# Optimization experiments

Hardware: AMD Instinct MI355X
Metric: run time of the kernel (lower is better)

Reference implementation:

```python
import jax, jax.numpy as jnp
from jax import lax
import numpy as np

I, H = 512, 1024
B, T = 64, 512


def setup_inputs() -> dict:
    key = jax.random.key(0)
    ks = jax.random.split(key, 16)
    p = lambda k, shape: (jax.random.normal(k, shape, dtype=jnp.float32) * 0.01)
    inp = {
        "inputs": jax.random.normal(ks[0], (B, T, I), dtype=jnp.float32),
        "h_prev_forward": jnp.zeros((B, H), dtype=jnp.float32),
        "h_prev_backward": jnp.zeros((B, H), dtype=jnp.float32),
        # forward-direction params
        "W_hr_f": p(ks[1], (H, H)), "W_xr_f": p(ks[2], (I, H)), "b_r_f": jnp.zeros((H,), jnp.float32),
        "W_hz_f": p(ks[3], (H, H)), "W_xz_f": p(ks[4], (I, H)), "b_z_f": jnp.zeros((H,), jnp.float32),
        "W_hh_f": p(ks[5], (H, H)), "W_xh_f": p(ks[6], (I, H)), "b_h_f": jnp.zeros((H,), jnp.float32),
        # backward-direction params
        "W_hr_b": p(ks[7], (H, H)), "W_xr_b": p(ks[8], (I, H)), "b_r_b": jnp.zeros((H,), jnp.float32),
        "W_hz_b": p(ks[9], (H, H)), "W_xz_b": p(ks[10], (I, H)), "b_z_b": jnp.zeros((H,), jnp.float32),
        "W_hh_b": p(ks[11], (H, H)), "W_xh_b": p(ks[12], (I, H)), "b_h_b": jnp.zeros((H,), jnp.float32),
    }
    return inp


def _gru_dir(x, h0, W_hr, W_xr, b_r, W_hz, W_xz, b_z, W_hh, W_xh, b_h, reverse):
    # Precompute input projections as big GEMMs: (B,T,I)@(I,H) -> (B,T,H)
    xr = jnp.einsum("bti,ih->bth", x, W_xr) + b_r
    xz = jnp.einsum("bti,ih->bth", x, W_xz) + b_z
    xh = jnp.einsum("bti,ih->bth", x, W_xh) + b_h
    # time-major for scan
    xs = (xr.transpose(1, 0, 2), xz.transpose(1, 0, 2), xh.transpose(1, 0, 2))

    def step(h, x_t):
        xr_t, xz_t, xh_t = x_t
        R = jax.nn.sigmoid(h @ W_hr + xr_t)
        Z = jax.nn.sigmoid(h @ W_hz + xz_t)
        # NOTE: original torch code computes (R * h) @ W_hh (left-to-right precedence)
        h_til = jnp.tanh((R * h) @ W_hh + xh_t)
        h_new = Z * h_til + (1.0 - Z) * h
        return h_new, h_new

    _, hs = lax.scan(step, h0, xs, reverse=reverse)  # hs: (T,B,H), time order preserved
    return hs.transpose(1, 0, 2)  # (B,T,H)


def reference(inputs, h_prev_forward, h_prev_backward,
              W_hr_f, W_xr_f, b_r_f, W_hz_f, W_xz_f, b_z_f, W_hh_f, W_xh_f, b_h_f,
              W_hr_b, W_xr_b, b_r_b, W_hz_b, W_xz_b, b_z_b, W_hh_b, W_xh_b, b_h_b):
    h_f = _gru_dir(inputs, h_prev_forward, W_hr_f, W_xr_f, b_r_f,
                   W_hz_f, W_xz_f, b_z_f, W_hh_f, W_xh_f, b_h_f, reverse=False)
    h_b = _gru_dir(inputs, h_prev_backward, W_hr_b, W_xr_b, b_r_b,
                   W_hz_b, W_xz_b, b_z_b, W_hh_b, W_xh_b, b_h_b, reverse=True)
    return jnp.concatenate([h_f, h_b], axis=2)  # (B,T,2H)
```

## Files before the change

kernel.cpp:

```cpp
#include <hip/hip_runtime.h>
#include <hip/hip_bf16.h>
#include <math.h>

typedef __bf16 bf16;
typedef __bf16 bf16x8 __attribute__((ext_vector_type(8)));
typedef __bf16 bf16x4 __attribute__((ext_vector_type(4)));
typedef float f32x4 __attribute__((ext_vector_type(4)));

#define T_LEN 512
#define BATCH 64
#define HDIM  1024
#define IDIM  512

struct Ptr12 { const float* p[12]; };
struct Ptr6  { const float* p[6];  };

__global__ __launch_bounds__(256) void transpose_convert(Ptr12 W, bf16* wt_h, bf16* wt_x) {
    int z = blockIdx.z;
    int K = (z < 6) ? HDIM : IDIM;
    const float* src = W.p[z];
    bf16* dst = (z < 6) ? (wt_h + (size_t)z * HDIM * HDIM)
                        : (wt_x + (size_t)(z - 6) * HDIM * IDIM);
    int n0 = blockIdx.x * 32;
    int k0 = blockIdx.y * 32;
    if (k0 >= K) return;
    __shared__ float tile[32][33];
    int tx = threadIdx.x & 31, ty = threadIdx.x >> 5;
#pragma unroll
    for (int i = 0; i < 32; i += 8)
        tile[ty + i][tx] = src[(size_t)(k0 + ty + i) * HDIM + n0 + tx];
    __syncthreads();
#pragma unroll
    for (int i = 0; i < 32; i += 8)
        dst[(size_t)(n0 + ty + i) * K + k0 + tx] = (bf16)tile[tx][ty + i];
}

__global__ __launch_bounds__(256) void convert_x(const float* __restrict__ x, bf16* __restrict__ xbf) {
    size_t i = ((size_t)blockIdx.x * blockDim.x + threadIdx.x) * 4;
    float4 v = *(const float4*)(x + i);
    bf16x4 o = { (bf16)v.x, (bf16)v.y, (bf16)v.z, (bf16)v.w };
    *(bf16x4*)(xbf + i) = o;
}

__global__ __launch_bounds__(256) void init_h(const float* __restrict__ hf, const float* __restrict__ hb,
                                              bf16* __restrict__ h_cur) {
    int i = blockIdx.x * blockDim.x + threadIdx.x;
    h_cur[i] = (bf16)hf[i];
    h_cur[BATCH * HDIM + i] = (bf16)hb[i];
}

__global__ __launch_bounds__(256) void xproj_gemm(const bf16* __restrict__ xbf,
                                                  const bf16* __restrict__ wt_x,
                                                  Ptr6 biases,
                                                  bf16* __restrict__ XP) {
    int g  = blockIdx.z;
    int m0 = blockIdx.x * 64;
    int n0 = blockIdx.y * 64;
    int w  = threadIdx.x >> 6;
    int l  = threadIdx.x & 63;
    int lm = l & 15, lq = l >> 4;

    const bf16* Wg    = wt_x + (size_t)g * HDIM * IDIM;
    const bf16* Abase = xbf + (size_t)(m0 + 16 * w + lm) * IDIM + lq * 8;
    const bf16* Bbase = Wg + (size_t)(n0 + lm) * IDIM + lq * 8;

    f32x4 acc[4] = {};
#pragma unroll 2
    for (int k = 0; k < IDIM; k += 32) {
        bf16x8 a = *(const bf16x8*)(Abase + k);
#pragma unroll
        for (int nt = 0; nt < 4; nt++) {
            bf16x8 b = *(const bf16x8*)(Bbase + (size_t)nt * 16 * IDIM + k);
            acc[nt] = __builtin_amdgcn_mfma_f32_16x16x32_bf16(a, b, acc[nt], 0, 0, 0);
        }
    }

    const float* bias = biases.p[g];
    int mrow = m0 + 16 * w + lq * 4;
#pragma unroll
    for (int nt = 0; nt < 4; nt++) {
        int n = n0 + nt * 16 + lm;
        float bv = bias[n];
#pragma unroll
        for (int r = 0; r < 4; r++) {
            int m = mrow + r;
            int b_ = m >> 9;
            int t  = m & 511;
            XP[(((size_t)g * T_LEN + t) * BATCH + b_) * HDIM + n] = (bf16)(acc[nt][r] + bv);
        }
    }
}

__global__ __launch_bounds__(256) void gru_phase_a(const bf16* __restrict__ wt_h,
                                                   const bf16* __restrict__ XP,
                                                   const bf16* __restrict__ h_cur,
                                                   bf16* __restrict__ Rh,
                                                   bf16* __restrict__ Zbuf,
                                                   int step) {
    int blk = blockIdx.x;
    int dir = blk >> 7;
    int gb  = (blk >> 6) & 1;
    int s   = blk & 63;
    int n0  = s * 16;
    int t   = dir ? (T_LEN - 1 - step) : step;

    int w = threadIdx.x >> 6, l = threadIdx.x & 63;
    int lm = l & 15, lq = l >> 4;
    int mt   = w & 1;
    int gate = w >> 1;
    int mrowA = gb * 32 + mt * 16 + lm;

    const bf16* h_d = h_cur + (size_t)dir * BATCH * HDIM;
    const bf16* Wp  = wt_h + (size_t)(dir * 3 + gate) * HDIM * HDIM + (size_t)(n0 + lm) * HDIM + lq * 8;
    const bf16* A   = h_d + (size_t)mrowA * HDIM + lq * 8;

    f32x4 acc = {};
#pragma unroll 8
    for (int k = 0; k < HDIM; k += 32) {
        bf16x8 a = *(const bf16x8*)(A + k);
        bf16x8 b = *(const bf16x8*)(Wp + k);
        acc = __builtin_amdgcn_mfma_f32_16x16x32_bf16(a, b, acc, 0, 0, 0);
    }

    const bf16* xp = XP + ((size_t)(dir * 3 + gate) * T_LEN + t) * BATCH * HDIM;
    int n = n0 + lm;
    int brow = gb * 32 + mt * 16 + lq * 4;
#pragma unroll
    for (int r = 0; r < 4; r++) {
        int b_ = brow + r;
        float pre = acc[r] + (float)xp[(size_t)b_ * HDIM + n];
        float gv = 1.0f / (1.0f + __expf(-pre));
        if (gate == 0) {
            float hv = (float)h_d[(size_t)b_ * HDIM + n];
            Rh[(size_t)dir * BATCH * HDIM + (size_t)b_ * HDIM + n] = (bf16)(gv * hv);
        } else {
            Zbuf[(size_t)dir * BATCH * HDIM + (size_t)b_ * HDIM + n] = (bf16)gv;
        }
    }
}

__global__ __launch_bounds__(128) void gru_phase_b(const bf16* __restrict__ wt_h,
                                                   const bf16* __restrict__ XP,
                                                   const bf16* __restrict__ Rh,
                                                   const bf16* __restrict__ Zbuf,
                                                   bf16* __restrict__ h_cur,
                                                   float* __restrict__ out,
                                                   int step) {
    int blk = blockIdx.x;
    int dir = blk >> 7;
    int gb  = (blk >> 6) & 1;
    int s   = blk & 63;
    int n0  = s * 16;
    int t   = dir ? (T_LEN - 1 - step) : step;

    int w = threadIdx.x >> 6, l = threadIdx.x & 63;
    int lm = l & 15, lq = l >> 4;
    int mrowA = gb * 32 + w * 16 + lm;

    const bf16* Rh_d = Rh + (size_t)dir * BATCH * HDIM;
    const bf16* Wp   = wt_h + (size_t)(dir * 3 + 2) * HDIM * HDIM + (size_t)(n0 + lm) * HDIM + lq * 8;
    const bf16* A    = Rh_d + (size_t)mrowA * HDIM + lq * 8;

    f32x4 acc = {};
#pragma unroll 8
    for (int k = 0; k < HDIM; k += 32) {
        bf16x8 a = *(const bf16x8*)(A + k);
        bf16x8 b = *(const bf16x8*)(Wp + k);
        acc = __builtin_amdgcn_mfma_f32_16x16x32_bf16(a, b, acc, 0, 0, 0);
    }

    bf16* h_d = h_cur + (size_t)dir * BATCH * HDIM;
    const bf16* Z_d = Zbuf + (size_t)dir * BATCH * HDIM;
    const bf16* xp = XP + ((size_t)(dir * 3 + 2) * T_LEN + t) * BATCH * HDIM;
    int n = n0 + lm;
    int brow = gb * 32 + w * 16 + lq * 4;
#pragma unroll
    for (int r = 0; r < 4; r++) {
        int b_ = brow + r;
        float pre = acc[r] + (float)xp[(size_t)b_ * HDIM + n];
        float e2x = __expf(2.0f * pre);
        float ht  = (e2x - 1.0f) / (e2x + 1.0f);
        float z   = (float)Z_d[(size_t)b_ * HDIM + n];
        float ho  = (float)h_d[(size_t)b_ * HDIM + n];
        float hn  = z * ht + (1.0f - z) * ho;
        h_d[(size_t)b_ * HDIM + n] = (bf16)hn;
        out[((size_t)b_ * T_LEN + t) * (2 * HDIM) + (size_t)dir * HDIM + n] = hn;
    }
}

extern "C" void kernel_launch(void* const* d_in, const int* in_sizes, int n_in,
                              void* d_out, int out_size, void* d_ws, size_t ws_size,
                              hipStream_t stream) {
    const float* x   = (const float*)d_in[0];
    const float* hpf = (const float*)d_in[1];
    const float* hpb = (const float*)d_in[2];

    unsigned char* ws = (unsigned char*)d_ws;
    size_t off = 0;
    bf16* wt_h = (bf16*)(ws + off); off += (size_t)6 * HDIM * HDIM * 2;
    bf16* wt_x = (bf16*)(ws + off); off += (size_t)6 * HDIM * IDIM * 2;
    bf16* xbf  = (bf16*)(ws + off); off += (size_t)BATCH * T_LEN * IDIM * 2;
    bf16* XP   = (bf16*)(ws + off); off += (size_t)6 * T_LEN * BATCH * HDIM * 2;
    bf16* h_cur = (bf16*)(ws + off); off += (size_t)2 * BATCH * HDIM * 2;
    bf16* Rh    = (bf16*)(ws + off); off += (size_t)2 * BATCH * HDIM * 2;
    bf16* Zbuf  = (bf16*)(ws + off); off += (size_t)2 * BATCH * HDIM * 2;

    float* out = (float*)d_out;

    Ptr12 wp;
    wp.p[0] = (const float*)d_in[3];  wp.p[1] = (const float*)d_in[6];  wp.p[2] = (const float*)d_in[9];
    wp.p[3] = (const float*)d_in[12]; wp.p[4] = (const float*)d_in[15]; wp.p[5] = (const float*)d_in[18];
    wp.p[6] = (const float*)d_in[4];  wp.p[7] = (const float*)d_in[7];  wp.p[8] = (const float*)d_in[10];
    wp.p[9] = (const float*)d_in[13]; wp.p[10] = (const float*)d_in[16]; wp.p[11] = (const float*)d_in[19];
    transpose_convert<<<dim3(32, 32, 12), 256, 0, stream>>>(wp, wt_h, wt_x);

    convert_x<<<16384, 256, 0, stream>>>(x, xbf);

    init_h<<<256, 256, 0, stream>>>(hpf, hpb, h_cur);

    Ptr6 bp;
    bp.p[0] = (const float*)d_in[5];  bp.p[1] = (const float*)d_in[8];  bp.p[2] = (const float*)d_in[11];
    bp.p[3] = (const float*)d_in[14]; bp.p[4] = (const float*)d_in[17]; bp.p[5] = (const float*)d_in[20];
    xproj_gemm<<<dim3(512, 16, 6), 256, 0, stream>>>(xbf, wt_x, bp, XP);

    for (int step = 0; step < T_LEN; ++step) {
        gru_phase_a<<<256, 256, 0, stream>>>(wt_h, XP, h_cur, Rh, Zbuf, step);
        gru_phase_b<<<256, 128, 0, stream>>>(wt_h, XP, Rh, Zbuf, h_cur, out, step);
    }
}
```

Before: 12.27 ms.

## Fuse the GRU recurrence into a persistent kernel with LDS-resident weights

Replaces the 1024 per-timestep launches of the two phase kernels with a single persistent kernel of 256 blocks. Each block loads its slice of the three recurrent weight matrices into shared memory once. Per-direction atomic grid barriers separate the gate phase from the candidate phase at every step. The update gate now stays in LDS instead of going through global memory. The candidate GEMM is also split over K across waves and reduced in LDS. This removes launch overhead and the repeated global weight reads. The cost is that all 256 blocks must be co-resident, and correctness depends on a spin barrier and on acquire/release visibility of the h and Rh buffers across blocks.

```diff
diff --git a/kernel.cpp b/kernel.cpp
--- a/kernel.cpp
+++ b/kernel.cpp
@@ -91,100 +91,120 @@
     }
 }
 
-__global__ __launch_bounds__(256) void gru_phase_a(const bf16* __restrict__ wt_h,
-                                                   const bf16* __restrict__ XP,
-                                                   const bf16* __restrict__ h_cur,
-                                                   bf16* __restrict__ Rh,
-                                                   bf16* __restrict__ Zbuf,
-                                                   int step) {
+__device__ __forceinline__ void dir_barrier(unsigned* ctr, unsigned target) {
+    __syncthreads();
+    if (threadIdx.x == 0) {
+        __hip_atomic_fetch_add(ctr, 1u, __ATOMIC_RELEASE, __HIP_MEMORY_SCOPE_AGENT);
+        while (__hip_atomic_load(ctr, __ATOMIC_ACQUIRE, __HIP_MEMORY_SCOPE_AGENT) < target)
+            __builtin_amdgcn_s_sleep(2);
+    }
+    __syncthreads();
+}
+
+__global__ __launch_bounds__(256, 1) void gru_persist(const bf16* __restrict__ wt_h,
+                                                      const bf16* __restrict__ XP,
+                                                      bf16* __restrict__ h_all,
+                                                      bf16* __restrict__ Rh_all,
+                                                      float* __restrict__ out,
+                                                      unsigned* __restrict__ bar) {
+    __shared__ bf16  Wlds[3 * 32 * 64 * 8];
+    __shared__ float Zlds[2][64][4];
+    __shared__ float Red[2][64][4];
+
     int blk = blockIdx.x;
     int dir = blk >> 7;
     int gb  = (blk >> 6) & 1;
     int s   = blk & 63;
     int n0  = s * 16;
-    int t   = dir ? (T_LEN - 1 - step) : step;
 
     int w = threadIdx.x >> 6, l = threadIdx.x & 63;
     int lm = l & 15, lq = l >> 4;
-    int mt   = w & 1;
-    int gate = w >> 1;
-    int mrowA = gb * 32 + mt * 16 + lm;
-
-    const bf16* h_d = h_cur + (size_t)dir * BATCH * HDIM;
-    const bf16* Wp  = wt_h + (size_t)(dir * 3 + gate) * HDIM * HDIM + (size_t)(n0 + lm) * HDIM + lq * 8;
-    const bf16* A   = h_d + (size_t)mrowA * HDIM + lq * 8;
-
-    f32x4 acc = {};
+
+    bf16* h_d  = h_all  + (size_t)dir * BATCH * HDIM;
+    bf16* Rh_d = Rh_all + (size_t)dir * BATCH * HDIM;
+    const bf16* Wsrc = wt_h + (size_t)dir * 3 * HDIM * HDIM;
+
+    for (int idx = threadIdx.x; idx < 3 * 32 * 64; idx += 256) {
+        int gate = idx >> 11;
+        int rem  = idx & 2047;
+        int kc   = rem >> 6;
+        int ln   = rem & 63;
+        int n    = n0 + (ln & 15);
+        int k    = kc * 32 + (ln >> 4) * 8;
+        *(bf16x8*)&Wlds[(size_t)idx * 8] =
+            *(const bf16x8*)(Wsrc + (size_t)gate * HDIM * HDIM + (size_t)n * HDIM + k);
+    }
+    __syncthreads();
+
+    unsigned* bar_d = bar + dir * 1024;
+
+    for (int step = 0; step < T_LEN; ++step) {
+        int t = dir ? (T_LEN - 1 - step) : step;
+
+        {
+            int gate = w >> 1, mt = w & 1;
+            int m0 = gb * 32 + mt * 16;
+            const bf16* A  = h_d + (size_t)(m0 + lm) * HDIM + lq * 8;
+            const bf16* Bl = &Wlds[((size_t)(gate * 32) * 64 + l) * 8];
+            f32x4 acc = {};
 #pragma unroll 8
-    for (int k = 0; k < HDIM; k += 32) {
-        bf16x8 a = *(const bf16x8*)(A + k);
-        bf16x8 b = *(const bf16x8*)(Wp + k);
-        acc = __builtin_amdgcn_mfma_f32_16x16x32_bf16(a, b, acc, 0, 0, 0);
-    }
-
-    const bf16* xp = XP + ((size_t)(dir * 3 + gate) * T_LEN + t) * BATCH * HDIM;
-    int n = n0 + lm;
-    int brow = gb * 32 + mt * 16 + lq * 4;
-#pragma unroll
-    for (int r = 0; r < 4; r++) {
-        int b_ = brow + r;
-        float pre = acc[r] + (float)xp[(size_t)b_ * HDIM + n];
-        float gv = 1.0f / (1.0f + __expf(-pre));
-        if (gate == 0) {
-            float hv = (float)h_d[(size_t)b_ * HDIM + n];
-            Rh[(size_t)dir * BATCH * HDIM + (size_t)b_ * HDIM + n] = (bf16)(gv * hv);
-        } else {
-            Zbuf[(size_t)dir * BATCH * HDIM + (size_t)b_ * HDIM + n] = (bf16)gv;
-        }
-    }
-}
-
-__global__ __launch_bounds__(128) void gru_phase_b(const bf16* __restrict__ wt_h,
-                                                   const bf16* __restrict__ XP,
-                                                   const bf16* __restrict__ Rh,
-                                                   const bf16* __restrict__ Zbuf,
-                                                   bf16* __restrict__ h_cur,
-                                                   float* __restrict__ out,
-                                                   int step) {
-    int blk = blockIdx.x;
-    int dir = blk >> 7;
-    int gb  = (blk >> 6) & 1;
-    int s   = blk & 63;
-    int n0  = s * 16;
-    int t   = dir ? (T_LEN - 1 - step) : step;
-
-    int w = threadIdx.x >> 6, l = threadIdx.x & 63;
-    int lm = l & 15, lq = l >> 4;
-    int mrowA = gb * 32 + w * 16 + lm;
-
-    const bf16* Rh_d = Rh + (size_t)dir * BATCH * HDIM;
-    const bf16* Wp   = wt_h + (size_t)(dir * 3 + 2) * HDIM * HDIM + (size_t)(n0 + lm) * HDIM + lq * 8;
-    const bf16* A    = Rh_d + (size_t)mrowA * HDIM + lq * 8;
-
-    f32x4 acc = {};
+            for (int kc = 0; kc < 32; ++kc) {
+                bf16x8 a = *(const bf16x8*)(A + kc * 32);
+                bf16x8 b = *(const bf16x8*)(Bl + (size_t)kc * 64 * 8);
+                acc = __builtin_amdgcn_mfma_f32_16x16x32_bf16(a, b, acc, 0, 0, 0);
+            }
+            const bf16* xp = XP + ((size_t)(dir * 3 + gate) * T_LEN + t) * BATCH * HDIM;
+            int n = n0 + lm;
+#pragma unroll
+            for (int r = 0; r < 4; ++r) {
+                int b_ = m0 + lq * 4 + r;
+                float pre = acc[r] + (float)xp[(size_t)b_ * HDIM + n];
+                float g = 1.0f / (1.0f + __expf(-pre));
+                if (gate == 0) {
+                    float hv = (float)h_d[(size_t)b_ * HDIM + n];
+                    Rh_d[(size_t)b_ * HDIM + n] = (bf16)(g * hv);
+                } else {
+                    Zlds[mt][l][r] = g;
+                }
+            }
+        }
+        dir_barrier(&bar_d[step * 2], 128u);
+
+        {
+            int mt = w & 1, kh = w >> 1;
+            int m0 = gb * 32 + mt * 16;
+            const bf16* A  = Rh_d + (size_t)(m0 + lm) * HDIM + kh * 512 + lq * 8;
+            const bf16* Bl = &Wlds[((size_t)(2 * 32 + kh * 16) * 64 + l) * 8];
+            f32x4 acc = {};
 #pragma unroll 8
-    for (int k = 0; k < HDIM; k += 32) {
-        bf16x8 a = *(const bf16x8*)(A + k);
-        bf16x8 b = *(const bf16x8*)(Wp + k);
-        acc = __builtin_amdgcn_mfma_f32_16x16x32_bf16(a, b, acc, 0, 0, 0);
-    }
-
-    bf16* h_d = h_cur + (size_t)dir * BATCH * HDIM;
-    const bf16* Z_d = Zbuf + (size_t)dir * BATCH * HDIM;
-    const bf16* xp = XP + ((size_t)(dir * 3 + 2) * T_LEN + t) * BATCH * HDIM;
-    int n = n0 + lm;
-    int brow = gb * 32 + w * 16 + lq * 4;
-#pragma unroll
-    for (int r = 0; r < 4; r++) {
-        int b_ = brow + r;
-        float pre = acc[r] + (float)xp[(size_t)b_ * HDIM + n];
-        float e2x = __expf(2.0f * pre);
-        float ht  = (e2x - 1.0f) / (e2x + 1.0f);
-        float z   = (float)Z_d[(size_t)b_ * HDIM + n];
-        float ho  = (float)h_d[(size_t)b_ * HDIM + n];
-        float hn  = z * ht + (1.0f - z) * ho;
-        h_d[(size_t)b_ * HDIM + n] = (bf16)hn;
-        out[((size_t)b_ * T_LEN + t) * (2 * HDIM) + (size_t)dir * HDIM + n] = hn;
+            for (int kc = 0; kc < 16; ++kc) {
+                bf16x8 a = *(const bf16x8*)(A + kc * 32);
+                bf16x8 b = *(const bf16x8*)(Bl + (size_t)kc * 64 * 8);
+                acc = __builtin_amdgcn_mfma_f32_16x16x32_bf16(a, b, acc, 0, 0, 0);
+            }
+            if (kh == 1) {
+#pragma unroll
+                for (int r = 0; r < 4; ++r) Red[mt][l][r] = acc[r];
+            }
+            __syncthreads();
+            if (kh == 0) {
+                const bf16* xp = XP + ((size_t)(dir * 3 + 2) * T_LEN + t) * BATCH * HDIM;
+                int n = n0 + lm;
+#pragma unroll
+                for (int r = 0; r < 4; ++r) {
+                    int b_ = m0 + lq * 4 + r;
+                    float pre = acc[r] + Red[mt][l][r] + (float)xp[(size_t)b_ * HDIM + n];
+                    float e2x = __expf(2.0f * pre);
+                    float ht  = (e2x - 1.0f) / (e2x + 1.0f);
+                    float z   = Zlds[mt][l][r];
+                    float ho  = (float)h_d[(size_t)b_ * HDIM + n];
+                    float hn  = z * ht + (1.0f - z) * ho;
+                    h_d[(size_t)b_ * HDIM + n] = (bf16)hn;
+                    out[((size_t)b_ * T_LEN + t) * (2 * HDIM) + (size_t)dir * HDIM + n] = hn;
+                }
+            }
+        }
+        dir_barrier(&bar_d[step * 2 + 1], 128u);
     }
 }
 
@@ -203,7 +223,7 @@
     bf16* XP   = (bf16*)(ws + off); off += (size_t)6 * T_LEN * BATCH * HDIM * 2;
     bf16* h_cur = (bf16*)(ws + off); off += (size_t)2 * BATCH * HDIM * 2;
     bf16* Rh    = (bf16*)(ws + off); off += (size_t)2 * BATCH * HDIM * 2;
-    bf16* Zbuf  = (bf16*)(ws + off); off += (size_t)2 * BATCH * HDIM * 2;
+    unsigned* bar = (unsigned*)(ws + off);
 
     float* out = (float*)d_out;
 
@@ -218,13 +238,12 @@
 
     init_h<<<256, 256, 0, stream>>>(hpf, hpb, h_cur);
 
+    hipMemsetAsync(bar, 0, 2 * 1024 * sizeof(unsigned), stream);
+
     Ptr6 bp;
     bp.p[0] = (const float*)d_in[5];  bp.p[1] = (const float*)d_in[8];  bp.p[2] = (const float*)d_in[11];
     bp.p[3] = (const float*)d_in[14]; bp.p[4] = (const float*)d_in[17]; bp.p[5] = (const float*)d_in[20];
     xproj_gemm<<<dim3(512, 16, 6), 256, 0, stream>>>(xbf, wt_x, bp, XP);
 
-    for (int step = 0; step < T_LEN; ++step) {
-        gru_phase_a<<<256, 256, 0, stream>>>(wt_h, XP, h_cur, Rh, Zbuf, step);
-        gru_phase_b<<<256, 128, 0, stream>>>(wt_h, XP, Rh, Zbuf, h_cur, out, step);
-    }
-}
+    gru_persist<<<256, 256, 0, stream>>>(wt_h, XP, h_cur, Rh, out, bar);
+}
```

Result: slower. 21.44 ms (+74.8%).
